# Kernel tuning notes

Hardware: AMD Instinct MI355X
Metric: run time of the kernel (lower is better)

## Reference

```python
import jax, jax.numpy as jnp
import numpy as np

L, D_IN, D_MODEL, N_LAYERS = 4096, 8, 256, 2
ED, N, K = 512, 16, 4          # d_inner = 2*d_model, d_state, d_conv
DT_RANK = 16                   # ceil(d_model/16)
EPS = 1e-5


def setup_inputs() -> dict:
    key = jax.random.key(0)
    ks = jax.random.split(key, 10)
    def g(k, shape, s=0.02):
        return jax.random.normal(k, shape, jnp.float32) * s
    A_init = jnp.tile(jnp.arange(1, N + 1, dtype=jnp.float32), (N_LAYERS, ED, 1))
    return {
        "x": jax.random.normal(ks[0], (L, D_IN), jnp.float32),
        "fc_in_w": g(ks[1], (D_MODEL, D_IN), 0.1),
        "fc_in_b": jnp.zeros((D_MODEL,), jnp.float32),
        "fc_out_w": g(ks[2], (1, D_MODEL), 0.1),
        "fc_out_b": jnp.zeros((1,), jnp.float32),
        "norm_w": jnp.ones((N_LAYERS, D_MODEL), jnp.float32),
        "in_proj_w": g(ks[3], (N_LAYERS, 2 * ED, D_MODEL)),
        "conv_w": g(ks[4], (N_LAYERS, ED, 1, K), 0.1),
        "conv_b": jnp.zeros((N_LAYERS, ED), jnp.float32),
        "x_proj_w": g(ks[5], (N_LAYERS, DT_RANK + 2 * N, ED)),
        "dt_proj_w": g(ks[6], (N_LAYERS, ED, DT_RANK), 0.1),
        "dt_proj_b": jnp.full((N_LAYERS, ED), -4.0, jnp.float32),  # softplus(-4)~0.018
        "A_log": jnp.log(A_init),
        "D": jnp.ones((N_LAYERS, ED), jnp.float32),
        "out_proj_w": g(ks[7], (N_LAYERS, D_MODEL, ED)),
    }


def rmsnorm(x, w):
    return x * jax.lax.rsqrt(jnp.mean(x * x, axis=-1, keepdims=True) + EPS) * w


def causal_depthwise_conv(x, w, b):
    # x: [L, ED], w: [ED, 1, K] -> causal depthwise conv along L
    y = jax.lax.conv_general_dilated(
        x.T[None],  # [1, ED, L]
        w, (1,), [(K - 1, 0)],
        dimension_numbers=("NCH", "OIH", "NCH"),
        feature_group_count=ED)
    return y[0].T + b  # [L, ED]


def mamba_block(x, p):
    norm_w, in_w, cw, cb, xp_w, dtw, dtb, a_log, d, out_w = p
    xn = rmsnorm(x, norm_w)
    xz = xn @ in_w.T                      # [L, 2*ED]
    xi, z = xz[:, :ED], xz[:, ED:]
    xc = jax.nn.silu(causal_depthwise_conv(xi, cw, cb))   # [L, ED]
    dbc = xc @ xp_w.T                     # [L, DT_RANK + 2N]
    delta = jax.nn.softplus(dbc[:, :DT_RANK] @ dtw.T + dtb)  # [L, ED]
    B = dbc[:, DT_RANK:DT_RANK + N]       # [L, N]
    C = dbc[:, DT_RANK + N:]              # [L, N]
    A = -jnp.exp(a_log)                   # [ED, N]
    dA = jnp.exp(delta[:, :, None] * A[None])                 # [L, ED, N]
    dBx = delta[:, :, None] * B[:, None, :] * xc[:, :, None]  # [L, ED, N]

    def step(h, inp):
        da, dbx, c = inp
        h = da * h + dbx                  # [ED, N]
        return h, jnp.einsum("en,n->e", h, c)

    _, ys = jax.lax.scan(step, jnp.zeros((ED, N), x.dtype), (dA, dBx, C))
    y = (ys + d * xc) * jax.nn.silu(z)
    return x + y @ out_w.T


def forward(x, fc_in_w, fc_in_b, fc_out_w, fc_out_b, norm_w, in_proj_w, conv_w,
            conv_b, x_proj_w, dt_proj_w, dt_proj_b, A_log, D, out_proj_w):
    h = x @ fc_in_w.T + fc_in_b           # [L, D_MODEL]

    def layer(h, p):
        return mamba_block(h, p), None

    h, _ = jax.lax.scan(layer, h, (norm_w, in_proj_w, conv_w, conv_b, x_proj_w,
                                   dt_proj_w, dt_proj_b, A_log, D, out_proj_w))
    out = jnp.tanh(h @ fc_out_w.T + fc_out_b)  # [L, 1]
    return out.reshape(-1)


def reference(x, fc_in_w, fc_in_b, fc_out_w, fc_out_b, norm_w, in_proj_w, conv_w,
              conv_b, x_proj_w, dt_proj_w, dt_proj_b, A_log, D, out_proj_w):
    return forward(x, fc_in_w, fc_in_b, fc_out_w, fc_out_b, norm_w, in_proj_w,
                   conv_w, conv_b, x_proj_w, dt_proj_w, dt_proj_b, A_log, D,
                   out_proj_w)
```

## Files before the change

kernel.cpp:

```cpp
#include <hip/hip_runtime.h>
#include <math.h>

#define LSEQ 4096
#define D_IN 8
#define D_MODEL 256
#define ED 512
#define NSTATE 16
#define KCONV 4
#define DT_RANK 16
#define EPS 1e-5f
#define NCHUNK 256
#define CHUNK 16

typedef short short8 __attribute__((ext_vector_type(8)));
typedef unsigned short ushort8 __attribute__((ext_vector_type(8)));
typedef float f32x4 __attribute__((ext_vector_type(4)));

__device__ __forceinline__ float sigmoidf_(float x){ return 1.f/(1.f+__expf(-x)); }
__device__ __forceinline__ float siluf_(float x){ return x*sigmoidf_(x); }
__device__ __forceinline__ float softplusf_(float x){
  return (x > 20.f) ? x : log1pf(__expf(x));
}
__device__ __forceinline__ unsigned short f2bf(float f){
  unsigned int u = __float_as_uint(f);
  return (unsigned short)((u + 0x7fffu + ((u>>16)&1u)) >> 16);
}

__global__ void k_prep(const float* __restrict__ x, const float* __restrict__ fiw,
                       const float* __restrict__ fib, const float* __restrict__ ipw,
                       const float* __restrict__ xpw, const float* __restrict__ opw,
                       float* __restrict__ h, unsigned short* __restrict__ wip,
                       unsigned short* __restrict__ wxp, unsigned short* __restrict__ wop){
  int b = blockIdx.x, tid = threadIdx.x;
  if (b < 2048) {
    int i = b*256 + tid;
    wip[i] = f2bf(ipw[i]);
    if (i < 2*48*ED)      wxp[i] = f2bf(xpw[i]);
    if (i < 2*D_MODEL*ED) wop[i] = f2bf(opw[i]);
  } else {
    int idx = (b-2048)*256 + tid;
    int t = idx >> 8, d = idx & 255;
    float acc = fib[d];
#pragma unroll
    for (int i = 0; i < D_IN; ++i) acc += x[t*D_IN+i]*fiw[d*D_IN+i];
    h[idx] = acc;
  }
}

template<int WM, int WN, bool RMS, bool ACC, bool ABF16>
__global__ __launch_bounds__(256) void k_gemm_mfma(
    const void* __restrict__ Ap, const unsigned short* __restrict__ B,
    float* __restrict__ C, int M, int N, int K, const float* __restrict__ nwp)
{
  constexpr int BM = 32*WM, BN = 32*WN, LDT = 40;
  const float* A = (const float*)Ap;
  const unsigned short* Ab = (const unsigned short*)Ap;
  __shared__ unsigned short As[BM*LDT];
  __shared__ unsigned short Bs[BN*LDT];
  __shared__ float rms_lds[BM];
  __shared__ float nws[D_MODEL];
  const int tid = threadIdx.x;
  const int bm = blockIdx.x*BM, bn = blockIdx.y*BN;
  const int w = tid >> 6, lane = tid & 63;
  const int mb = (w>>1)*WM*16, nb = (w&1)*WN*16;
  const int lr = lane & 15, lk = (lane>>4)*8;
  if (RMS) {
    nws[tid] = nwp[tid];
    int row = tid >> 1, half = tid & 1;
    const float* ap = A + (size_t)(bm+row)*K + half*128;
    float s = 0.f;
#pragma unroll
    for (int i = 0; i < 128; i += 4) {
      float4 v = *(const float4*)&ap[i];
      s += v.x*v.x + v.y*v.y + v.z*v.z + v.w*v.w;
    }
    s += __shfl_xor(s, 1);
    if (!half) rms_lds[row] = rsqrtf(s*(1.f/D_MODEL) + EPS);
    __syncthreads();
  }
  f32x4 acc[WM][WN] = {};
  for (int k0 = 0; k0 < K; k0 += 32) {
#pragma unroll 2
    for (int s = tid; s < BM*4; s += 256) {
      int row = s>>2, kg = (s&3)*8;
      if (ABF16) {
        *(ushort8*)&As[row*LDT+kg] = *(const ushort8*)&Ab[(size_t)(bm+row)*K + k0 + kg];
      } else {
        const float* ap = &A[(size_t)(bm+row)*K + k0 + kg];
        float4 a0 = *(const float4*)ap, a1 = *(const float4*)(ap+4);
        if (RMS) {
          float rs = rms_lds[row];
          a0.x *= rs*nws[k0+kg+0]; a0.y *= rs*nws[k0+kg+1];
          a0.z *= rs*nws[k0+kg+2]; a0.w *= rs*nws[k0+kg+3];
          a1.x *= rs*nws[k0+kg+4]; a1.y *= rs*nws[k0+kg+5];
          a1.z *= rs*nws[k0+kg+6]; a1.w *= rs*nws[k0+kg+7];
        }
        ushort8 o;
        o[0]=f2bf(a0.x); o[1]=f2bf(a0.y); o[2]=f2bf(a0.z); o[3]=f2bf(a0.w);
        o[4]=f2bf(a1.x); o[5]=f2bf(a1.y); o[6]=f2bf(a1.z); o[7]=f2bf(a1.w);
        *(ushort8*)&As[row*LDT+kg] = o;
      }
    }
#pragma unroll 2
    for (int s = tid; s < BN*4; s += 256) {
      int row = s>>2, kg = (s&3)*8;
      ushort8 v = {0,0,0,0,0,0,0,0};
      if (bn+row < N) v = *(const ushort8*)&B[(size_t)(bn+row)*K + k0 + kg];
      *(ushort8*)&Bs[row*LDT+kg] = v;
    }
    __syncthreads();
    short8 af[WM], bfr[WN];
#pragma unroll
    for (int i = 0; i < WM; ++i) af[i]  = *(const short8*)&As[(mb+i*16+lr)*LDT + lk];
#pragma unroll
    for (int j = 0; j < WN; ++j) bfr[j] = *(const short8*)&Bs[(nb+j*16+lr)*LDT + lk];
#pragma unroll
    for (int i = 0; i < WM; ++i)
#pragma unroll
      for (int j = 0; j < WN; ++j)
        acc[i][j] = __builtin_amdgcn_mfma_f32_16x16x32_bf16(af[i], bfr[j], acc[i][j], 0, 0, 0);
    __syncthreads();
  }
#pragma unroll
  for (int i = 0; i < WM; ++i) {
#pragma unroll
    for (int j = 0; j < WN; ++j) {
      int col = bn + nb + j*16 + lr;
      if (col < N) {
#pragma unroll
        for (int r = 0; r < 4; ++r) {
          int row = bm + mb + i*16 + (lane>>4)*4 + r;
          size_t o = (size_t)row*N + col;
          C[o] = ACC ? (C[o] + acc[i][j][r]) : acc[i][j][r];
        }
      }
    }
  }
}

__global__ __launch_bounds__(512) void k_cxps1(
    const float* __restrict__ xz, const float* __restrict__ cw, const float* __restrict__ cb,
    const unsigned short* __restrict__ wxp, const float* __restrict__ dtw,
    const float* __restrict__ dtb, const float* __restrict__ alog,
    float* __restrict__ xc, float* __restrict__ dbc,
    float* __restrict__ S, float* __restrict__ Q)
{
  constexpr int LDA = ED + 8;
  __shared__ unsigned short As[CHUNK*LDA];
  __shared__ float Ds[CHUNK][DT_RANK];
  __shared__ float Bsh[CHUNK][NSTATE];
  const int tid = threadIdx.x;
  const int e = tid;
  const int c = blockIdx.x;
  const int t0 = c*CHUNK;
  float cwv[KCONV];
#pragma unroll
  for (int k = 0; k < KCONV; ++k) cwv[k] = cw[e*KCONV+k];
  float cbv = cb[e];
  float w0=0.f, w1=0.f, w2=0.f;
  if (t0 > 0) {
    w0 = xz[(size_t)(t0-3)*(2*ED) + e];
    w1 = xz[(size_t)(t0-2)*(2*ED) + e];
    w2 = xz[(size_t)(t0-1)*(2*ED) + e];
  }
  float xv[CHUNK];
#pragma unroll
  for (int t = 0; t < CHUNK; ++t) {
    float cur = xz[(size_t)(t0+t)*(2*ED) + e];
    float v = siluf_(cbv + w0*cwv[0] + w1*cwv[1] + w2*cwv[2] + cur*cwv[3]);
    xv[t] = v;
    xc[(size_t)(t0+t)*ED + e] = v;
    w0=w1; w1=w2; w2=cur;
  }
#pragma unroll
  for (int t = 0; t < CHUNK; ++t) {
    unsigned int us = f2bf(xv[t]);
    unsigned int other = (unsigned int)__shfl_down((int)us, 1);
    if ((tid & 1) == 0) *(unsigned int*)&As[t*LDA + e] = us | (other << 16);
  }
  __syncthreads();
  const int w = tid >> 6, lane = tid & 63;
  const int lr = lane & 15, lk = (lane>>4)*8;
  if (w < 3) {
    f32x4 acc = {};
#pragma unroll
    for (int ks = 0; ks < ED/32; ++ks) {
      short8 af = *(const short8*)&As[lr*LDA + ks*32 + lk];
      short8 bf = *(const short8*)&wxp[(size_t)(w*16+lr)*ED + ks*32 + lk];
      acc = __builtin_amdgcn_mfma_f32_16x16x32_bf16(af, bf, acc, 0, 0, 0);
    }
#pragma unroll
    for (int r = 0; r < 4; ++r) {
      int row = (lane>>4)*4 + r;
      dbc[(size_t)(t0+row)*48 + w*16 + lr] = acc[r];
      if (w == 0) Ds[row][lr] = acc[r];
      else if (w == 1) Bsh[row][lr] = acc[r];
    }
  }
  __syncthreads();
  float dtwv[DT_RANK];
#pragma unroll
  for (int r = 0; r < DT_RANK; ++r) dtwv[r] = dtw[e*DT_RANK+r];
  float dtbv = dtb[e];
  float A[NSTATE], h[NSTATE];
#pragma unroll
  for (int n = 0; n < NSTATE; ++n) { A[n] = -__expf(alog[e*NSTATE+n]); h[n] = 0.f; }
  float sd = 0.f;
#pragma unroll
  for (int t = 0; t < CHUNK; ++t) {
    float da = dtbv;
#pragma unroll
    for (int r = 0; r < DT_RANK; ++r) da += Ds[t][r]*dtwv[r];
    float d = softplusf_(da);
    sd += d;
    float dx = d*xv[t];
#pragma unroll
    for (int n = 0; n < NSTATE; ++n)
      h[n] = __expf(d*A[n])*h[n] + dx*Bsh[t][n];
  }
  S[(size_t)c*ED + e] = sd;
#pragma unroll
  for (int n = 0; n < NSTATE; ++n) Q[(size_t)(c*NSTATE+n)*ED + e] = h[n];
}

__global__ __launch_bounds__(256) void k_scan2(
    const float* __restrict__ alog, const float* __restrict__ S, float* __restrict__ Q)
{
  __shared__ float Pl[8][32], Rl[8][32], Hs[8][32];
  const int tid = threadIdx.x;
  const int seg = tid >> 5, chl = tid & 31;
  const int ch = blockIdx.x*32 + chl;
  const int n = ch >> 9, e = ch & 511;
  const float a = -__expf(alog[e*NSTATE+n]);
  const int c0 = seg*32;
  float ev[32], qv[32];
#pragma unroll
  for (int k = 0; k < 32; ++k) ev[k] = S[(size_t)(c0+k)*ED + e];
#pragma unroll
  for (int k = 0; k < 32; ++k) qv[k] = Q[(size_t)((c0+k)*NSTATE+n)*ED + e];
#pragma unroll
  for (int k = 0; k < 32; ++k) ev[k] = __expf(a*ev[k]);
  float P = 1.f, R = 0.f;
#pragma unroll
  for (int k = 0; k < 32; ++k) { R = ev[k]*R + qv[k]; P *= ev[k]; }
  Pl[seg][chl] = P; Rl[seg][chl] = R;
  __syncthreads();
  if (tid < 32) {
    float hcur = 0.f;
#pragma unroll
    for (int s = 0; s < 8; ++s) { Hs[s][tid] = hcur; hcur = Pl[s][tid]*hcur + Rl[s][tid]; }
  }
  __syncthreads();
  float h = Hs[seg][chl];
#pragma unroll
  for (int k = 0; k < 32; ++k) {
    Q[(size_t)((c0+k)*NSTATE+n)*ED + e] = h;
    h = ev[k]*h + qv[k];
  }
}

__global__ __launch_bounds__(512) void k_scan3(
    const float* __restrict__ xc, const float* __restrict__ dbc,
    const float* __restrict__ dtw, const float* __restrict__ dtb,
    const float* __restrict__ alog, const float* __restrict__ Hin,
    const float* __restrict__ xz, const float* __restrict__ Dv,
    unsigned short* __restrict__ y)
{
  __shared__ float Ds[CHUNK][DT_RANK];
  __shared__ float Bsh[CHUNK][NSTATE];
  __shared__ float Cs[CHUNK][NSTATE];
  const int tid = threadIdx.x;
  const int e = tid;
  const int c = blockIdx.x;
  const int t0 = c*CHUNK;
  for (int i = tid; i < CHUNK*48; i += 512) {
    int t = i/48, col = i - t*48;
    float v = dbc[(size_t)(t0+t)*48 + col];
    if (col < DT_RANK) Ds[t][col] = v;
    else if (col < DT_RANK+NSTATE) Bsh[t][col-DT_RANK] = v;
    else Cs[t][col-DT_RANK-NSTATE] = v;
  }
  __syncthreads();
  float dtwv[DT_RANK];
#pragma unroll
  for (int r = 0; r < DT_RANK; ++r) dtwv[r] = dtw[e*DT_RANK+r];
  float dtbv = dtb[e];
  float x[CHUNK], z[CHUNK];
#pragma unroll
  for (int t = 0; t < CHUNK; ++t) x[t] = xc[(size_t)(t0+t)*ED + e];
#pragma unroll
  for (int t = 0; t < CHUNK; ++t) z[t] = xz[(size_t)(t0+t)*(2*ED) + ED + e];
  float A[NSTATE], h[NSTATE];
#pragma unroll
  for (int n = 0; n < NSTATE; ++n) {
    A[n] = -__expf(alog[e*NSTATE+n]);
    h[n] = Hin[(size_t)(c*NSTATE+n)*ED + e];
  }
  float dv = Dv[e];
#pragma unroll
  for (int t = 0; t < CHUNK; ++t) {
    float da = dtbv;
#pragma unroll
    for (int r = 0; r < DT_RANK; ++r) da += Ds[t][r]*dtwv[r];
    float d = softplusf_(da);
    float dx = d*x[t];
    float ysum = 0.f;
#pragma unroll
    for (int n = 0; n < NSTATE; ++n) {
      h[n] = __expf(d*A[n])*h[n] + dx*Bsh[t][n];
      ysum += h[n]*Cs[t][n];
    }
    y[(size_t)(t0+t)*ED + e] = f2bf((ysum + dv*x[t]) * siluf_(z[t]));
  }
}

__global__ void k_fc_out(const float* __restrict__ h, const float* __restrict__ w,
                         const float* __restrict__ b, float* __restrict__ out){
  int wave = threadIdx.x >> 6, lane = threadIdx.x & 63;
  int row = blockIdx.x*4 + wave;
  const float4 hv = *(const float4*)&h[row*D_MODEL + lane*4];
  const float4 wv = *(const float4*)&w[lane*4];
  float s = hv.x*wv.x + hv.y*wv.y + hv.z*wv.z + hv.w*wv.w;
#pragma unroll
  for (int m = 32; m; m >>= 1) s += __shfl_xor(s, m);
  if (lane == 0) out[row] = tanhf(s + b[0]);
}

extern "C" void kernel_launch(void* const* d_in, const int* in_sizes, int n_in,
                              void* d_out, int out_size, void* d_ws, size_t ws_size,
                              hipStream_t stream){
  const float* x    = (const float*)d_in[0];
  const float* fiw  = (const float*)d_in[1];
  const float* fib  = (const float*)d_in[2];
  const float* fow  = (const float*)d_in[3];
  const float* fob  = (const float*)d_in[4];
  const float* nw   = (const float*)d_in[5];
  const float* ipw  = (const float*)d_in[6];
  const float* cw   = (const float*)d_in[7];
  const float* cb   = (const float*)d_in[8];
  const float* xpw  = (const float*)d_in[9];
  const float* dtw  = (const float*)d_in[10];
  const float* dtb  = (const float*)d_in[11];
  const float* alog = (const float*)d_in[12];
  const float* Dv   = (const float*)d_in[13];
  const float* opw  = (const float*)d_in[14];

  float* W = (float*)d_ws;
  float* h   = W;
  float* xz  = h   + (size_t)LSEQ*D_MODEL;
  float* xc  = xz  + (size_t)LSEQ*2*ED;
  float* dbc = xc  + (size_t)LSEQ*ED;
  float* S   = dbc + (size_t)LSEQ*48;
  float* Q   = S   + (size_t)NCHUNK*ED;
  unsigned short* yb  = (unsigned short*)(Q + (size_t)NCHUNK*NSTATE*ED);
  unsigned short* wip = yb  + (size_t)LSEQ*ED;
  unsigned short* wxp = wip + (size_t)2*2*ED*D_MODEL;
  unsigned short* wop = wxp + (size_t)2*48*ED;

  k_prep<<<2048 + LSEQ, 256, 0, stream>>>(x, fiw, fib, ipw, xpw, opw, h, wip, wxp, wop);

  for (int l = 0; l < 2; ++l) {
    const unsigned short* wip_l = wip + (size_t)l*2*ED*D_MODEL;
    const unsigned short* wxp_l = wxp + (size_t)l*48*ED;
    const unsigned short* wop_l = wop + (size_t)l*D_MODEL*ED;
    const float* nw_l   = nw   + l*D_MODEL;
    const float* cw_l   = cw   + l*ED*KCONV;
    const float* cb_l   = cb   + l*ED;
    const float* dtw_l  = dtw  + l*ED*DT_RANK;
    const float* dtb_l  = dtb  + l*ED;
    const float* alog_l = alog + l*ED*NSTATE;
    const float* D_l    = Dv   + l*ED;

    k_gemm_mfma<4,4,true,false,false><<<dim3(LSEQ/128, (2*ED)/128), 256, 0, stream>>>(
        h, wip_l, xz, LSEQ, 2*ED, D_MODEL, nw_l);
    k_cxps1<<<NCHUNK, 512, 0, stream>>>(xz, cw_l, cb_l, wxp_l, dtw_l, dtb_l, alog_l,
                                        xc, dbc, S, Q);
    k_scan2<<<NCHUNK, 256, 0, stream>>>(alog_l, S, Q);
    k_scan3<<<NCHUNK, 512, 0, stream>>>(xc, dbc, dtw_l, dtb_l, alog_l, Q, xz, D_l, yb);
    k_gemm_mfma<2,2,false,true,true><<<dim3(LSEQ/64, D_MODEL/64), 256, 0, stream>>>(
        yb, wop_l, h, LSEQ, D_MODEL, ED, nullptr);
  }

  k_fc_out<<<LSEQ/4, 256, 0, stream>>>(h, fow, fob, (float*)d_out);
}
```

Baseline: 184.9 us.

## Store xz and chunk states in bf16 and recompute conv in scan3

The in_proj GEMM now writes xz as bf16, and the chunk-state buffer Q passed between scan kernels is stored as bf16. The xc intermediate is no longer written: k_scan3 recomputes the causal conv and SiLU from xz. The aim is to cut global memory traffic between the stages. The cost is lower precision in xz and in the inter-chunk states, plus some redundant conv arithmetic.

Result: no change. 185.3 us (+0.2%).

```diff
diff --git a/kernel.cpp b/kernel.cpp
--- a/kernel.cpp
+++ b/kernel.cpp
@@ -24,6 +24,9 @@
 __device__ __forceinline__ unsigned short f2bf(float f){
   unsigned int u = __float_as_uint(f);
   return (unsigned short)((u + 0x7fffu + ((u>>16)&1u)) >> 16);
+}
+__device__ __forceinline__ float bf2f(unsigned short u){
+  return __uint_as_float(((unsigned int)u) << 16);
 }
 
 __global__ void k_prep(const float* __restrict__ x, const float* __restrict__ fiw,
@@ -47,14 +50,16 @@
   }
 }
 
-template<int WM, int WN, bool RMS, bool ACC, bool ABF16>
+template<int WM, int WN, bool RMS, bool ACC, bool ABF16, bool CBF16>
 __global__ __launch_bounds__(256) void k_gemm_mfma(
     const void* __restrict__ Ap, const unsigned short* __restrict__ B,
-    float* __restrict__ C, int M, int N, int K, const float* __restrict__ nwp)
+    void* __restrict__ Cp, int M, int N, int K, const float* __restrict__ nwp)
 {
   constexpr int BM = 32*WM, BN = 32*WN, LDT = 40;
   const float* A = (const float*)Ap;
   const unsigned short* Ab = (const unsigned short*)Ap;
+  float* Cf = (float*)Cp;
+  unsigned short* Cb = (unsigned short*)Cp;
   __shared__ unsigned short As[BM*LDT];
   __shared__ unsigned short Bs[BN*LDT];
   __shared__ float rms_lds[BM];
@@ -131,7 +136,9 @@
         for (int r = 0; r < 4; ++r) {
           int row = bm + mb + i*16 + (lane>>4)*4 + r;
           size_t o = (size_t)row*N + col;
-          C[o] = ACC ? (C[o] + acc[i][j][r]) : acc[i][j][r];
+          if (CBF16)      Cb[o] = f2bf(acc[i][j][r]);
+          else if (ACC)   Cf[o] = Cf[o] + acc[i][j][r];
+          else            Cf[o] = acc[i][j][r];
         }
       }
     }
@@ -139,11 +146,11 @@
 }
 
 __global__ __launch_bounds__(512) void k_cxps1(
-    const float* __restrict__ xz, const float* __restrict__ cw, const float* __restrict__ cb,
-    const unsigned short* __restrict__ wxp, const float* __restrict__ dtw,
-    const float* __restrict__ dtb, const float* __restrict__ alog,
-    float* __restrict__ xc, float* __restrict__ dbc,
-    float* __restrict__ S, float* __restrict__ Q)
+    const unsigned short* __restrict__ xzb, const float* __restrict__ cw,
+    const float* __restrict__ cb, const unsigned short* __restrict__ wxp,
+    const float* __restrict__ dtw, const float* __restrict__ dtb,
+    const float* __restrict__ alog, float* __restrict__ dbc,
+    float* __restrict__ S, unsigned short* __restrict__ Q)
 {
   constexpr int LDA = ED + 8;
   __shared__ unsigned short As[CHUNK*LDA];
@@ -159,17 +166,16 @@
   float cbv = cb[e];
   float w0=0.f, w1=0.f, w2=0.f;
   if (t0 > 0) {
-    w0 = xz[(size_t)(t0-3)*(2*ED) + e];
-    w1 = xz[(size_t)(t0-2)*(2*ED) + e];
-    w2 = xz[(size_t)(t0-1)*(2*ED) + e];
+    w0 = bf2f(xzb[(size_t)(t0-3)*(2*ED) + e]);
+    w1 = bf2f(xzb[(size_t)(t0-2)*(2*ED) + e]);
+    w2 = bf2f(xzb[(size_t)(t0-1)*(2*ED) + e]);
   }
   float xv[CHUNK];
 #pragma unroll
   for (int t = 0; t < CHUNK; ++t) {
-    float cur = xz[(size_t)(t0+t)*(2*ED) + e];
+    float cur = bf2f(xzb[(size_t)(t0+t)*(2*ED) + e]);
     float v = siluf_(cbv + w0*cwv[0] + w1*cwv[1] + w2*cwv[2] + cur*cwv[3]);
     xv[t] = v;
-    xc[(size_t)(t0+t)*ED + e] = v;
     w0=w1; w1=w2; w2=cur;
   }
 #pragma unroll
@@ -220,11 +226,12 @@
   }
   S[(size_t)c*ED + e] = sd;
 #pragma unroll
-  for (int n = 0; n < NSTATE; ++n) Q[(size_t)(c*NSTATE+n)*ED + e] = h[n];
+  for (int n = 0; n < NSTATE; ++n) Q[(size_t)(c*NSTATE+n)*ED + e] = f2bf(h[n]);
 }
 
 __global__ __launch_bounds__(256) void k_scan2(
-    const float* __restrict__ alog, const float* __restrict__ S, float* __restrict__ Q)
+    const float* __restrict__ alog, const float* __restrict__ S,
+    unsigned short* __restrict__ Q)
 {
   __shared__ float Pl[8][32], Rl[8][32], Hs[8][32];
   const int tid = threadIdx.x;
@@ -237,7 +244,7 @@
 #pragma unroll
   for (int k = 0; k < 32; ++k) ev[k] = S[(size_t)(c0+k)*ED + e];
 #pragma unroll
-  for (int k = 0; k < 32; ++k) qv[k] = Q[(size_t)((c0+k)*NSTATE+n)*ED + e];
+  for (int k = 0; k < 32; ++k) qv[k] = bf2f(Q[(size_t)((c0+k)*NSTATE+n)*ED + e]);
 #pragma unroll
   for (int k = 0; k < 32; ++k) ev[k] = __expf(a*ev[k]);
   float P = 1.f, R = 0.f;
@@ -254,17 +261,18 @@
   float h = Hs[seg][chl];
 #pragma unroll
   for (int k = 0; k < 32; ++k) {
-    Q[(size_t)((c0+k)*NSTATE+n)*ED + e] = h;
-    h = ev[k]*h + qv[k];
+    float hl = qv[k];
+    Q[(size_t)((c0+k)*NSTATE+n)*ED + e] = f2bf(h);
+    h = ev[k]*h + hl;
   }
 }
 
 __global__ __launch_bounds__(512) void k_scan3(
-    const float* __restrict__ xc, const float* __restrict__ dbc,
+    const unsigned short* __restrict__ xzb, const float* __restrict__ dbc,
+    const float* __restrict__ cw, const float* __restrict__ cb,
     const float* __restrict__ dtw, const float* __restrict__ dtb,
-    const float* __restrict__ alog, const float* __restrict__ Hin,
-    const float* __restrict__ xz, const float* __restrict__ Dv,
-    unsigned short* __restrict__ y)
+    const float* __restrict__ alog, const unsigned short* __restrict__ Hin,
+    const float* __restrict__ Dv, unsigned short* __restrict__ y)
 {
   __shared__ float Ds[CHUNK][DT_RANK];
   __shared__ float Bsh[CHUNK][NSTATE];
@@ -280,21 +288,35 @@
     else if (col < DT_RANK+NSTATE) Bsh[t][col-DT_RANK] = v;
     else Cs[t][col-DT_RANK-NSTATE] = v;
   }
+  float cwv[KCONV];
+#pragma unroll
+  for (int k = 0; k < KCONV; ++k) cwv[k] = cw[e*KCONV+k];
+  float cbv = cb[e];
+  float w0=0.f, w1=0.f, w2=0.f;
+  if (t0 > 0) {
+    w0 = bf2f(xzb[(size_t)(t0-3)*(2*ED) + e]);
+    w1 = bf2f(xzb[(size_t)(t0-2)*(2*ED) + e]);
+    w2 = bf2f(xzb[(size_t)(t0-1)*(2*ED) + e]);
+  }
+  float x[CHUNK], z[CHUNK];
+#pragma unroll
+  for (int t = 0; t < CHUNK; ++t) {
+    float cur = bf2f(xzb[(size_t)(t0+t)*(2*ED) + e]);
+    x[t] = siluf_(cbv + w0*cwv[0] + w1*cwv[1] + w2*cwv[2] + cur*cwv[3]);
+    w0=w1; w1=w2; w2=cur;
+  }
+#pragma unroll
+  for (int t = 0; t < CHUNK; ++t) z[t] = bf2f(xzb[(size_t)(t0+t)*(2*ED) + ED + e]);
   __syncthreads();
   float dtwv[DT_RANK];
 #pragma unroll
   for (int r = 0; r < DT_RANK; ++r) dtwv[r] = dtw[e*DT_RANK+r];
   float dtbv = dtb[e];
-  float x[CHUNK], z[CHUNK];
-#pragma unroll
-  for (int t = 0; t < CHUNK; ++t) x[t] = xc[(size_t)(t0+t)*ED + e];
-#pragma unroll
-  for (int t = 0; t < CHUNK; ++t) z[t] = xz[(size_t)(t0+t)*(2*ED) + ED + e];
   float A[NSTATE], h[NSTATE];
 #pragma unroll
   for (int n = 0; n < NSTATE; ++n) {
     A[n] = -__expf(alog[e*NSTATE+n]);
-    h[n] = Hin[(size_t)(c*NSTATE+n)*ED + e];
+    h[n] = bf2f(Hin[(size_t)(c*NSTATE+n)*ED + e]);
   }
   float dv = Dv[e];
 #pragma unroll
@@ -347,12 +369,11 @@
 
   float* W = (float*)d_ws;
   float* h   = W;
-  float* xz  = h   + (size_t)LSEQ*D_MODEL;
-  float* xc  = xz  + (size_t)LSEQ*2*ED;
-  float* dbc = xc  + (size_t)LSEQ*ED;
+  float* dbc = h   + (size_t)LSEQ*D_MODEL;
   float* S   = dbc + (size_t)LSEQ*48;
-  float* Q   = S   + (size_t)NCHUNK*ED;
-  unsigned short* yb  = (unsigned short*)(Q + (size_t)NCHUNK*NSTATE*ED);
+  unsigned short* xzb = (unsigned short*)(S + (size_t)NCHUNK*ED);
+  unsigned short* Q   = xzb + (size_t)LSEQ*2*ED;
+  unsigned short* yb  = Q   + (size_t)NCHUNK*NSTATE*ED;
   unsigned short* wip = yb  + (size_t)LSEQ*ED;
   unsigned short* wxp = wip + (size_t)2*2*ED*D_MODEL;
   unsigned short* wop = wxp + (size_t)2*48*ED;
@@ -371,13 +392,14 @@
     const float* alog_l = alog + l*ED*NSTATE;
     const float* D_l    = Dv   + l*ED;
 
-    k_gemm_mfma<4,4,true,false,false><<<dim3(LSEQ/128, (2*ED)/128), 256, 0, stream>>>(
-        h, wip_l, xz, LSEQ, 2*ED, D_MODEL, nw_l);
-    k_cxps1<<<NCHUNK, 512, 0, stream>>>(xz, cw_l, cb_l, wxp_l, dtw_l, dtb_l, alog_l,
-                                        xc, dbc, S, Q);
+    k_gemm_mfma<4,4,true,false,false,true><<<dim3(LSEQ/128, (2*ED)/128), 256, 0, stream>>>(
+        h, wip_l, xzb, LSEQ, 2*ED, D_MODEL, nw_l);
+    k_cxps1<<<NCHUNK, 512, 0, stream>>>(xzb, cw_l, cb_l, wxp_l, dtw_l, dtb_l, alog_l,
+                                        dbc, S, Q);
     k_scan2<<<NCHUNK, 256, 0, stream>>>(alog_l, S, Q);
-    k_scan3<<<NCHUNK, 512, 0, stream>>>(xc, dbc, dtw_l, dtb_l, alog_l, Q, xz, D_l, yb);
-    k_gemm_mfma<2,2,false,true,true><<<dim3(LSEQ/64, D_MODEL/64), 256, 0, stream>>>(
+    k_scan3<<<NCHUNK, 512, 0, stream>>>(xzb, dbc, cw_l, cb_l, dtw_l, dtb_l, alog_l,
+                                        Q, D_l, yb);
+    k_gemm_mfma<2,2,false,true,true,false><<<dim3(LSEQ/64, D_MODEL/64), 256, 0, stream>>>(
         yb, wop_l, h, LSEQ, D_MODEL, ED, nullptr);
   }
 
```
